# Performance work log

Measured on AMD Instinct MI355X. Metric: run time of the kernel, lower is better.

Reference implementation:

```python
import jax, jax.numpy as jnp
import numpy as np

N_NODES = 100000
N_EDGES = 1600000
N_GRAPHS = 1024
DIM_IN = 128
DIM_SELF = 16
BN_EPS = 1e-5


def _bn(x, gamma, beta):
    # training-mode BatchNorm1d over dim 0 (biased variance, as torch uses for normalization)
    m = jnp.mean(x, axis=0)
    v = jnp.mean((x - m) ** 2, axis=0)
    return gamma * (x - m) * jax.lax.rsqrt(v + BN_EPS) + beta


def _mlp(x, W1, b1, g, b, W2, b2):
    h = x @ W1 + b1
    h = jax.nn.relu(_bn(h, g, b))
    return h @ W2 + b2


def _gin(h, src, dst, W1, b1, g, b, W2, b2):
    # GINConv with eps=0: (1+eps)*h + sum over in-neighbors, then MLP
    agg = jax.ops.segment_sum(h[src], dst, num_segments=N_NODES)
    return _mlp(h + agg, W1, b1, g, b, W2, b2)


def setup_inputs() -> dict:
    key = jax.random.key(0)
    ks = jax.random.split(key, 16)

    def lin(k, fan_in, fan_out):
        bound = 1.0 / np.sqrt(fan_in)
        k1, k2 = jax.random.split(k)
        W = jax.random.uniform(k1, (fan_in, fan_out), jnp.float32, -bound, bound)
        b = jax.random.uniform(k2, (fan_out,), jnp.float32, -bound, bound)
        return W, b

    inp = {}
    inp['feat'] = jax.random.normal(ks[0], (N_NODES, DIM_IN), jnp.float32)
    inp['self_feat'] = jax.random.normal(ks[1], (N_GRAPHS, DIM_SELF), jnp.float32)
    inp['edge_src'] = jax.random.randint(ks[2], (N_EDGES,), 0, N_NODES, jnp.int32)
    inp['edge_dst'] = jax.random.randint(ks[3], (N_EDGES,), 0, N_NODES, jnp.int32)
    inp['node2graph'] = jnp.sort(jax.random.randint(ks[4], (N_NODES,), 0, N_GRAPHS, jnp.int32))

    inp['g1_W1'], inp['g1_b1'] = lin(ks[5], DIM_IN, 100)
    inp['g1_gamma'] = jnp.ones((100,), jnp.float32)
    inp['g1_beta'] = jnp.zeros((100,), jnp.float32)
    inp['g1_W2'], inp['g1_b2'] = lin(ks[6], 100, 100)

    inp['g2_W1'], inp['g2_b1'] = lin(ks[7], 100, 20)
    inp['g2_gamma'] = jnp.ones((20,), jnp.float32)
    inp['g2_beta'] = jnp.zeros((20,), jnp.float32)
    inp['g2_W2'], inp['g2_b2'] = lin(ks[8], 20, 20)

    inp['fc1_W'], inp['fc1_b'] = lin(ks[9], 20 * DIM_SELF, 32)
    inp['bn1_gamma'] = jnp.ones((32,), jnp.float32)
    inp['bn1_beta'] = jnp.zeros((32,), jnp.float32)
    inp['fc2_W'], inp['fc2_b'] = lin(ks[10], 32, 8)
    inp['bn2_gamma'] = jnp.ones((8,), jnp.float32)
    inp['bn2_beta'] = jnp.zeros((8,), jnp.float32)
    inp['fc3_W'], inp['fc3_b'] = lin(ks[11], 8, 1)
    return inp


def reference(feat, self_feat,
              g1_W1, g1_b1, g1_gamma, g1_beta, g1_W2, g1_b2,
              g2_W1, g2_b1, g2_gamma, g2_beta, g2_W2, g2_b2,
              fc1_W, fc1_b, bn1_gamma, bn1_beta,
              fc2_W, fc2_b, bn2_gamma, bn2_beta,
              fc3_W, fc3_b,
              edge_src, edge_dst, node2graph):
    h = _gin(feat, edge_src, edge_dst, g1_W1, g1_b1, g1_gamma, g1_beta, g1_W2, g1_b2)
    h = jax.nn.relu(h)
    h = _gin(h, edge_src, edge_dst, g2_W1, g2_b1, g2_gamma, g2_beta, g2_W2, g2_b2)
    h = jax.nn.relu(h)  # [N, 20]

    # dgl.mean_nodes: per-graph mean of node features
    sums = jax.ops.segment_sum(h, node2graph, num_segments=N_GRAPHS)  # [B, 20]
    cnts = jax.ops.segment_sum(jnp.ones((N_NODES,), h.dtype), node2graph, num_segments=N_GRAPHS)
    hg = sums / jnp.maximum(cnts, 1.0)[:, None]

    # kronecker fusion: bmm([B,20,1],[B,1,dim_self]) -> flatten
    kron = jnp.einsum('bi,bj->bij', hg, self_feat).reshape(N_GRAPHS, -1)  # [B, 20*dim_self]

    out = jax.nn.relu(_bn(kron @ fc1_W + fc1_b, bn1_gamma, bn1_beta))
    # dropout(0.3) is identity in eval mode
    out = jax.nn.relu(_bn(out @ fc2_W + fc2_b, bn2_gamma, bn2_beta))
    out = out @ fc3_W + fc3_b  # [B, dim_out]
    return out
```

## Files before the change

kernel.cpp:

```cpp
#include <hip/hip_runtime.h>

#define NN 100000
#define NE 1600000
#define NG 1024
#define DIN 128
#define D1 100
#define D2 20
#define DSELF 16
#define BN_EPS 1e-5f

#define NB 391
#define NBLK 782
#define EPB 2048
#define RAWCAP 5120
#define NAGG2 4000
#define NF1 25
#define NF2 40
#define APITCH 136

typedef unsigned int uint;
typedef unsigned short ushort;
typedef __attribute__((ext_vector_type(8))) short bfv8;
typedef __attribute__((ext_vector_type(4))) float fv4;

__device__ inline float bflo(uint x) { return __uint_as_float(x << 16); }
__device__ inline float bfhi(uint x) { return __uint_as_float(x & 0xffff0000u); }
__device__ inline uint packbf2(float a, float b) {
    uint ua = __float_as_uint(a), ub = __float_as_uint(b);
    ua += 0x7fffu + ((ua >> 16) & 1u);
    ub += 0x7fffu + ((ub >> 16) & 1u);
    return (ua >> 16) | (ub & 0xffff0000u);
}
__device__ inline ushort bfr(float x) {
    uint u = __float_as_uint(x);
    u += 0x7fffu + ((u >> 16) & 1u);
    return (ushort)(u >> 16);
}

__global__ __launch_bounds__(256) void k_gemm1(const float* __restrict__ feat,
                                               const float* __restrict__ W1,
                                               ushort* __restrict__ z1bf) {
    __shared__ __align__(16) char smem[64 * APITCH * 2 + 112 * APITCH * 2];
    ushort* Al = (ushort*)smem;
    ushort* Bt = (ushort*)(smem + 64 * APITCH * 2);
    int t = threadIdx.x;
    int row0 = blockIdx.x * 64;
#pragma unroll
    for (int i = 0; i < 8; i++) {
        int p = i * 256 + t;
        int r = p >> 5, cq = p & 31;
        int row = row0 + r; if (row >= NN) row = NN - 1;
        float4 v = *(const float4*)(feat + (size_t)row * DIN + cq * 4);
        ushort* dst = Al + r * APITCH + 4 * cq;
        dst[0] = bfr(v.x); dst[1] = bfr(v.y); dst[2] = bfr(v.z); dst[3] = bfr(v.w);
    }
    for (int p = t; p < 12800; p += 256) {
        int k = p / 100, n = p % 100;
        Bt[n * APITCH + k] = bfr(W1[p]);
    }
    __syncthreads();
    int w = __builtin_amdgcn_readfirstlane(t >> 6);
    int l = t & 63;
    int m16 = l & 15, quad = l >> 4;
    fv4 acc[7];
#pragma unroll
    for (int nt = 0; nt < 7; nt++) acc[nt] = (fv4){0.f, 0.f, 0.f, 0.f};
    const ushort* arow = Al + (w * 16 + m16) * APITCH;
#pragma unroll
    for (int kk = 0; kk < 4; kk++) {
        int kb = kk * 32 + quad * 8;
        bfv8 a = *(const bfv8*)(arow + kb);
#pragma unroll
        for (int nt = 0; nt < 7; nt++) {
            bfv8 b = *(const bfv8*)(Bt + (nt * 16 + m16) * APITCH + kb);
            acc[nt] = __builtin_amdgcn_mfma_f32_16x16x32_bf16(a, b, acc[nt], 0, 0, 0);
        }
    }
    __syncthreads();
    float* Ep = (float*)smem;
#pragma unroll
    for (int nt = 0; nt < 7; nt++) {
        int n = nt * 16 + m16;
        if (n < 100) {
#pragma unroll
            for (int rix = 0; rix < 4; rix++)
                Ep[(w * 16 + quad * 4 + rix) * 101 + n] = acc[nt][rix];
        }
    }
    __syncthreads();
#pragma unroll
    for (int i = 0; i < 13; i++) {
        int p = i * 256 + t;
        if (p < 3200) {
            int rr = p / 50, cc = 2 * (p % 50);
            int row = row0 + rr;
            if (row < NN) {
                float v0 = Ep[rr * 101 + cc], v1 = Ep[rr * 101 + cc + 1];
                *(uint*)(z1bf + (size_t)row * 128 + cc) = packbf2(v0, v1);
            }
        }
    }
}

__global__ __launch_bounds__(256) void k_csrA1(const int* __restrict__ dst,
                                               int* __restrict__ pbcount) {
    __shared__ int h[NB];
    int t = threadIdx.x, blk = blockIdx.x;
    for (int i = t; i < NB; i += 256) h[i] = 0;
    __syncthreads();
    int e0 = blk * EPB + t;
#pragma unroll
    for (int i = 0; i < 8; i++) {
        int e = e0 + i * 256;
        if (e < NE) atomicAdd(&h[dst[e] >> 8], 1);
    }
    __syncthreads();
    for (int i = t; i < NB; i += 256) pbcount[i * NBLK + blk] = h[i];
}

__global__ __launch_bounds__(1024) void k_csrS1(int* __restrict__ pbcount,
                                                int* __restrict__ btot) {
    __shared__ int s[1024];
    int t = threadIdx.x, b = blockIdx.x;
    int v = (t < NBLK) ? pbcount[b * NBLK + t] : 0;
    s[t] = v;
    __syncthreads();
    for (int off = 1; off < 1024; off <<= 1) {
        int x = (t >= off) ? s[t - off] : 0;
        __syncthreads();
        s[t] += x;
        __syncthreads();
    }
    if (t < NBLK) pbcount[b * NBLK + t] = s[t] - v;
    if (t == 1023) btot[b] = s[t];
}

__global__ __launch_bounds__(512) void k_csrS2(const int* __restrict__ btot,
                                               int* __restrict__ ebase) {
    __shared__ int s[512];
    int t = threadIdx.x;
    int v = (t < NB) ? btot[t] : 0;
    s[t] = v;
    __syncthreads();
    for (int off = 1; off < 512; off <<= 1) {
        int x = (t >= off) ? s[t - off] : 0;
        __syncthreads();
        s[t] += x;
        __syncthreads();
    }
    if (t < NB) ebase[t] = s[t] - v;
    if (t == NB - 1) ebase[NB] = s[t];
}

__global__ __launch_bounds__(256) void k_csrA2(const int* __restrict__ src,
                                               const int* __restrict__ dst,
                                               const int* __restrict__ pbexcl,
                                               const int* __restrict__ ebase,
                                               uint* __restrict__ gbuf) {
    __shared__ int cur[NB];
    int t = threadIdx.x, blk = blockIdx.x;
    for (int i = t; i < NB; i += 256) cur[i] = ebase[i] + pbexcl[i * NBLK + blk];
    __syncthreads();
    int e0 = blk * EPB + t;
#pragma unroll
    for (int i = 0; i < 8; i++) {
        int e = e0 + i * 256;
        if (e < NE) {
            int d = dst[e];
            int b = d >> 8;
            int pos = atomicAdd(&cur[b], 1);
            gbuf[pos] = (uint)src[e] | ((uint)(d & 255) << 17);
        }
    }
}

__global__ __launch_bounds__(256) void k_csrB(const uint* __restrict__ gbuf,
                                              const int* __restrict__ ebase,
                                              int* __restrict__ deg,
                                              int* __restrict__ offs,
                                              int* __restrict__ srcS) {
    __shared__ uint raw[RAWCAP];
    __shared__ int srt[RAWCAP];
    __shared__ int pref[256], cur[256];
    int t = threadIdx.x, b = blockIdx.x;
    int e0 = ebase[b], e1 = ebase[b + 1];
    int cnt = e1 - e0; if (cnt > RAWCAP) cnt = RAWCAP;
    cur[t] = 0;
    for (int i = t; i < cnt; i += 256) raw[i] = gbuf[e0 + i];
    __syncthreads();
    for (int i = t; i < cnt; i += 256) atomicAdd(&cur[raw[i] >> 17], 1);
    __syncthreads();
    int v = cur[t];
    pref[t] = v;
    __syncthreads();
    for (int off = 1; off < 256; off <<= 1) {
        int x = (t >= off) ? pref[t - off] : 0;
        __syncthreads();
        pref[t] += x;
        __syncthreads();
    }
    int excl = pref[t] - v;
    int node = b * 256 + t;
    if (node < NN) { deg[node] = v; offs[node] = e0 + excl; }
    cur[t] = excl;
    __syncthreads();
    for (int i = t; i < cnt; i += 256) {
        uint p = raw[i];
        int lpos = atomicAdd(&cur[p >> 17], 1);
        srt[lpos] = (int)(p & 0x1FFFFu);
    }
    __syncthreads();
    for (int i = t; i < cnt; i += 256) srcS[e0 + i] = srt[i];
}

__global__ __launch_bounds__(256) void k_agg1(const ushort* __restrict__ z1bf,
                                              const int* __restrict__ offs,
                                              const int* __restrict__ deg,
                                              const int* __restrict__ srcS,
                                              ushort* __restrict__ u1b) {
    int wq = __builtin_amdgcn_readfirstlane(threadIdx.x >> 6);
    int l = threadIdx.x & 63;
    int n = blockIdx.x * 4 + wq;
    if (n >= NN) return;
    int d = deg[n], base = offs[n];
    bool act = l < 50;
    const ushort* zc = z1bf + 2 * l;
    float a0 = 0.f, a1 = 0.f, b0 = 0.f, b1 = 0.f;
    float c0 = 0.f, c1 = 0.f, e0 = 0.f, e1 = 0.f;
    int i = 0;
    for (; i + 4 <= d; i += 4) {
        int s0 = srcS[base + i],     s1 = srcS[base + i + 1];
        int s2 = srcS[base + i + 2], s3 = srcS[base + i + 3];
        if (act) {
            uint x0 = *(const uint*)(zc + (size_t)s0 * 128);
            uint x1 = *(const uint*)(zc + (size_t)s1 * 128);
            uint x2 = *(const uint*)(zc + (size_t)s2 * 128);
            uint x3 = *(const uint*)(zc + (size_t)s3 * 128);
            a0 += bflo(x0); a1 += bfhi(x0);
            b0 += bflo(x1); b1 += bfhi(x1);
            c0 += bflo(x2); c1 += bfhi(x2);
            e0 += bflo(x3); e1 += bfhi(x3);
        }
    }
    for (; i < d; i++) {
        int s0 = srcS[base + i];
        if (act) {
            uint x0 = *(const uint*)(zc + (size_t)s0 * 128);
            a0 += bflo(x0); a1 += bfhi(x0);
        }
    }
    if (act) {
        uint xs = *(const uint*)(zc + (size_t)n * 128);
        float r0 = (a0 + b0) + (c0 + e0) + bflo(xs);
        float r1 = (a1 + b1) + (c1 + e1) + bfhi(xs);
        *(uint*)(u1b + (size_t)n * 100 + 2 * l) = packbf2(r0, r1);
    }
}

__global__ __launch_bounds__(256) void k_bnstat100(const ushort* __restrict__ u1b,
                                                   float* __restrict__ pb) {
    __shared__ float ls[10][100], lq[10][100];
    int t = threadIdx.x;
    int r0 = blockIdx.x * 200;
    int r1 = r0 + 200; if (r1 > NN) r1 = NN;
    if (t < 250) {
        int sub = t / 25, q = t % 25;
        float4 S = make_float4(0, 0, 0, 0), Q = make_float4(0, 0, 0, 0);
        for (int r = r0 + sub; r < r1; r += 10) {
            uint2 x = *(const uint2*)(u1b + (size_t)r * 100 + 4 * q);
            float v0 = bflo(x.x), v1 = bfhi(x.x), v2 = bflo(x.y), v3 = bfhi(x.y);
            S.x += v0; S.y += v1; S.z += v2; S.w += v3;
            Q.x = fmaf(v0, v0, Q.x); Q.y = fmaf(v1, v1, Q.y);
            Q.z = fmaf(v2, v2, Q.z); Q.w = fmaf(v3, v3, Q.w);
        }
        ls[sub][4 * q + 0] = S.x; ls[sub][4 * q + 1] = S.y;
        ls[sub][4 * q + 2] = S.z; ls[sub][4 * q + 3] = S.w;
        lq[sub][4 * q + 0] = Q.x; lq[sub][4 * q + 1] = Q.y;
        lq[sub][4 * q + 2] = Q.z; lq[sub][4 * q + 3] = Q.w;
    }
    __syncthreads();
    if (t < 100) {
        float S = 0.f, Q = 0.f;
#pragma unroll
        for (int s = 0; s < 10; s++) { S += ls[s][t]; Q += lq[s][t]; }
        pb[blockIdx.x * 200 + t] = S;
        pb[blockIdx.x * 200 + 100 + t] = Q;
    }
}

__global__ __launch_bounds__(256) void k_fold100(const float* __restrict__ pb,
                                                 float* __restrict__ pbf) {
    __shared__ float ls[4000];
    int t = threadIdx.x, b = blockIdx.x;
    for (int i = t; i < 4000; i += 256) ls[i] = pb[b * 4000 + i];
    __syncthreads();
    if (t < 200) {
        float S = 0.f;
#pragma unroll
        for (int j = 0; j < 20; j++) S += ls[j * 200 + t];
        pbf[b * 200 + t] = S;
    }
}

__global__ __launch_bounds__(512) void k_bnfin100(const float* __restrict__ pbf,
                                                  const float* __restrict__ gamma,
                                                  const float* __restrict__ beta,
                                                  float* __restrict__ sc,
                                                  float* __restrict__ sh) {
    __shared__ float ls[4][100], lq[4][100];
    int t = threadIdx.x;
    if (t < 400) {
        int sub = t / 100, c = t % 100;
        float S = 0.f, Q = 0.f;
        for (int b = sub; b < NF1; b += 4) {
            S += pbf[b * 200 + c];
            Q += pbf[b * 200 + 100 + c];
        }
        ls[sub][c] = S; lq[sub][c] = Q;
    }
    __syncthreads();
    if (t < 100) {
        float S = ls[0][t] + ls[1][t] + ls[2][t] + ls[3][t];
        float Q = lq[0][t] + lq[1][t] + lq[2][t] + lq[3][t];
        float mean = S * (1.f / NN);
        float var = Q * (1.f / NN) - mean * mean;
        float inv = rsqrtf(var + BN_EPS);
        float s = gamma[t] * inv;
        sc[t] = s;
        sh[t] = beta[t] - mean * s;
    }
}

__global__ __launch_bounds__(256) void k_m2(const ushort* __restrict__ u1b,
                                            const float* __restrict__ sc,
                                            const float* __restrict__ sh,
                                            const float* __restrict__ W2,
                                            const float* __restrict__ b2,
                                            const float* __restrict__ W1p,
                                            ushort* __restrict__ z2bf) {
    __shared__ float Xs[100 * 65];
    int t = threadIdx.x;
    int row0 = blockIdx.x * 64;
#pragma unroll
    for (int i = 0; i < 13; i++) {
        int p = i * 256 + t;
        if (p < 3200) {
            int r = p / 50, c = 2 * (p % 50);
            int row = row0 + r; if (row >= NN) row = NN - 1;
            uint x = *(const uint*)(u1b + (size_t)row * 100 + c);
            Xs[c * 65 + r] = fmaxf(bflo(x) * sc[c] + sh[c], 0.f);
            Xs[(c + 1) * 65 + r] = fmaxf(bfhi(x) * sc[c + 1] + sh[c + 1], 0.f);
        }
    }
    __syncthreads();
    int cg = __builtin_amdgcn_readfirstlane(t >> 6);
    int r = t & 63;
    int j0 = cg * 25;
    float H[25];
#pragma unroll
    for (int m = 0; m < 25; m++) H[m] = 0.f;
    for (int k = 0; k < D1; k++) {
        float a = Xs[k * 65 + r];
        const float* wr = W2 + k * D1 + j0;
#pragma unroll
        for (int m = 0; m < 25; m++) H[m] = fmaf(a, wr[m], H[m]);
    }
#pragma unroll
    for (int m = 0; m < 25; m++) H[m] = fmaxf(H[m] + b2[j0 + m], 0.f);
    float pz[20];
#pragma unroll
    for (int c = 0; c < 20; c++) pz[c] = 0.f;
#pragma unroll
    for (int m = 0; m < 25; m++) {
        const float* wp = W1p + (j0 + m) * D2;
#pragma unroll
        for (int c = 0; c < 20; c++) pz[c] = fmaf(H[m], wp[c], pz[c]);
    }
    __syncthreads();
    float* red = Xs;
#pragma unroll
    for (int c = 0; c < 20; c++) red[t * 20 + c] = pz[c];
    __syncthreads();
#pragma unroll
    for (int i = 0; i < 3; i++) {
        int p = i * 256 + t;
        if (p < 640) {
            int rr = p / 10, c2 = 2 * (p % 10);
            int row = row0 + rr;
            if (row < NN) {
                float v0 = red[rr * 20 + c2] + red[(64 + rr) * 20 + c2] +
                           red[(128 + rr) * 20 + c2] + red[(192 + rr) * 20 + c2];
                float v1 = red[rr * 20 + c2 + 1] + red[(64 + rr) * 20 + c2 + 1] +
                           red[(128 + rr) * 20 + c2 + 1] + red[(192 + rr) * 20 + c2 + 1];
                *(uint*)(z2bf + (size_t)row * 32 + c2) = packbf2(v0, v1);
            }
        }
    }
}

__global__ __launch_bounds__(256) void k_agg2(const ushort* __restrict__ z2bf,
                                              const int* __restrict__ offs,
                                              const int* __restrict__ deg,
                                              const int* __restrict__ srcS,
                                              float* __restrict__ u2,
                                              float* __restrict__ pb) {
    __shared__ float ls[500], lq[500];
    int t = threadIdx.x;
    int n = blockIdx.x * 25 + t / 10;
    int c2 = 2 * (t % 10);
    float r0 = 0.f, r1 = 0.f;
    if (t < 250 && n < NN) {
        int d = deg[n], base = offs[n];
        const ushort* zc = z2bf + c2;
        float a0 = 0.f, a1 = 0.f, b0 = 0.f, b1 = 0.f;
        int i = 0;
        for (; i + 2 <= d; i += 2) {
            uint x0 = *(const uint*)(zc + (size_t)srcS[base + i] * 32);
            uint x1 = *(const uint*)(zc + (size_t)srcS[base + i + 1] * 32);
            a0 += bflo(x0); a1 += bfhi(x0);
            b0 += bflo(x1); b1 += bfhi(x1);
        }
        if (i < d) {
            uint x0 = *(const uint*)(zc + (size_t)srcS[base + i] * 32);
            a0 += bflo(x0); a1 += bfhi(x0);
        }
        uint xs = *(const uint*)(zc + (size_t)n * 32);
        r0 = a0 + b0 + bflo(xs);
        r1 = a1 + b1 + bfhi(xs);
        *(float2*)(u2 + (size_t)n * D2 + c2) = make_float2(r0, r1);
    }
    if (t < 250) {
        int idx = (t / 10) * 20 + c2;
        ls[idx] = r0;     lq[idx] = r0 * r0;
        ls[idx + 1] = r1; lq[idx + 1] = r1 * r1;
    }
    __syncthreads();
    if (t < 20) {
        float S = 0.f, Q = 0.f;
#pragma unroll
        for (int j = 0; j < 25; j++) { S += ls[j * 20 + t]; Q += lq[j * 20 + t]; }
        pb[blockIdx.x * 40 + t] = S;
        pb[blockIdx.x * 40 + 20 + t] = Q;
    }
}

__global__ __launch_bounds__(256) void k_fold20(const float* __restrict__ pb,
                                                float* __restrict__ pbf) {
    __shared__ float ls[4000];
    int t = threadIdx.x, b = blockIdx.x;
    for (int i = t; i < 4000; i += 256) ls[i] = pb[b * 4000 + i];
    __syncthreads();
    if (t < 40) {
        float S = 0.f;
#pragma unroll
        for (int j = 0; j < 100; j++) S += ls[j * 40 + t];
        pbf[b * 40 + t] = S;
    }
}

__global__ __launch_bounds__(512) void k_bnfin20(const float* __restrict__ pbf,
                                                 const float* __restrict__ gamma,
                                                 const float* __restrict__ beta,
                                                 float* __restrict__ sc,
                                                 float* __restrict__ sh) {
    __shared__ float ls[25][20], lq[25][20];
    int t = threadIdx.x;
    if (t < 500) {
        int sub = t / 20, c = t % 20;
        float S = 0.f, Q = 0.f;
        for (int b = sub; b < NF2; b += 25) {
            S += pbf[b * 40 + c];
            Q += pbf[b * 40 + 20 + c];
        }
        ls[sub][c] = S; lq[sub][c] = Q;
    }
    __syncthreads();
    if (t < 20) {
        float S = 0.f, Q = 0.f;
#pragma unroll
        for (int s = 0; s < 25; s++) { S += ls[s][t]; Q += lq[s][t]; }
        float mean = S * (1.f / NN);
        float var = Q * (1.f / NN) - mean * mean;
        float inv = rsqrtf(var + BN_EPS);
        float s = gamma[t] * inv;
        sc[t] = s;
        sh[t] = beta[t] - mean * s;
    }
}

__global__ __launch_bounds__(256) void k_m3(const float* __restrict__ u2,
                                            const float* __restrict__ sc,
                                            const float* __restrict__ sh,
                                            const float* __restrict__ W2p,
                                            const float* __restrict__ b2p,
                                            float* __restrict__ h2) {
    int row = blockIdx.x * 256 + threadIdx.x;
    if (row >= NN) return;
    float ya[20];
    const float4* up = (const float4*)(u2 + (size_t)row * D2);
#pragma unroll
    for (int i = 0; i < 5; i++) {
        float4 v = up[i];
        float4 S = *(const float4*)(sc + 4 * i);
        float4 H = *(const float4*)(sh + 4 * i);
        ya[4 * i + 0] = fmaxf(v.x * S.x + H.x, 0.f);
        ya[4 * i + 1] = fmaxf(v.y * S.y + H.y, 0.f);
        ya[4 * i + 2] = fmaxf(v.z * S.z + H.z, 0.f);
        ya[4 * i + 3] = fmaxf(v.w * S.w + H.w, 0.f);
    }
    float hrow[D2];
#pragma unroll
    for (int j = 0; j < D2; j++) {
        float h = b2p[j];
#pragma unroll
        for (int k = 0; k < D2; k++) h = fmaf(ya[k], W2p[k * D2 + j], h);
        hrow[j] = fmaxf(h, 0.f);
    }
    float* hr = h2 + (size_t)row * D2;
#pragma unroll
    for (int c = 0; c < D2; c += 4) {
        float4 o; o.x = hrow[c]; o.y = hrow[c + 1]; o.z = hrow[c + 2]; o.w = hrow[c + 3];
        *(float4*)(hr + c) = o;
    }
}

__global__ __launch_bounds__(256) void k_pool(const float* __restrict__ h2,
                                              const int* __restrict__ n2g,
                                              float* __restrict__ hg) {
    int wq = __builtin_amdgcn_readfirstlane(threadIdx.x >> 6);
    int l = threadIdx.x & 63;
    int g = blockIdx.x * 4 + wq;
    if (g >= NG) return;
    int lo = 0, hi = NN;
    while (lo < hi) { int mid = (lo + hi) >> 1; if (n2g[mid] < g) lo = mid + 1; else hi = mid; }
    int s0 = lo;
    hi = NN;
    while (lo < hi) { int mid = (lo + hi) >> 1; if (n2g[mid] < g + 1) lo = mid + 1; else hi = mid; }
    int s1 = lo;
    float a = 0.f;
    if (l < 60) {
        int rg = l / 20, c = l % 20;
        for (int n = s0 + rg; n < s1; n += 3) a += h2[(size_t)n * D2 + c];
    }
    float v1 = __shfl(a, l + 20, 64);
    float v2 = __shfl(a, l + 40, 64);
    if (l < 20) {
        float cnt = (float)(s1 - s0);
        hg[g * D2 + l] = (a + v1 + v2) / fmaxf(cnt, 1.f);
    }
}

__global__ void k_head1(const float* __restrict__ hg, const float* __restrict__ sf,
                        const float* __restrict__ fc1W, float* __restrict__ a1) {
    int b = blockIdx.x * 8 + threadIdx.x / 32;
    int c = threadIdx.x % 32;
    if (b >= NG) return;
    const float* hgb = hg + b * D2;
    const float* sfb = sf + b * DSELF;
    float acc = 0.f;
    for (int i = 0; i < D2; i++) {
        float hi = hgb[i];
#pragma unroll
        for (int j = 0; j < DSELF; j++)
            acc += hi * sfb[j] * fc1W[(i * DSELF + j) * 32 + c];
    }
    a1[b * 32 + c] = acc;
}

__global__ __launch_bounds__(1024) void k_head2(
    const float* __restrict__ a1, const float* __restrict__ g1,
    const float* __restrict__ be1, const float* __restrict__ fc2W,
    const float* __restrict__ g2, const float* __restrict__ be2,
    const float* __restrict__ fc3W, const float* __restrict__ fc3b,
    float* __restrict__ out) {
    int t = threadIdx.x;
    int lane = t & 63, w = t >> 6;
    __shared__ float s1[16][32], s2[16][32];
    __shared__ float sc[32], sh[32], sc2[8], sh2[8];
    float x[32];
    const float4* ap = (const float4*)(a1 + t * 32);
#pragma unroll
    for (int i = 0; i < 8; i++) {
        float4 v = ap[i];
        x[4 * i] = v.x; x[4 * i + 1] = v.y; x[4 * i + 2] = v.z; x[4 * i + 3] = v.w;
    }
#pragma unroll
    for (int c = 0; c < 32; c++) {
        float v = x[c], q = v * v;
        for (int o = 32; o > 0; o >>= 1) {
            v += __shfl_down(v, o, 64);
            q += __shfl_down(q, o, 64);
        }
        if (lane == 0) { s1[w][c] = v; s2[w][c] = q; }
    }
    __syncthreads();
    if (t < 32) {
        float s = 0.f, q = 0.f;
        for (int ww = 0; ww < 16; ww++) { s += s1[ww][t]; q += s2[ww][t]; }
        float mean = s * (1.f / NG);
        float var = q * (1.f / NG) - mean * mean;
        float inv = rsqrtf(var + BN_EPS);
        float scl = g1[t] * inv;
        sc[t] = scl;
        sh[t] = be1[t] - mean * scl;
    }
    __syncthreads();
#pragma unroll
    for (int c = 0; c < 32; c++) x[c] = fmaxf(x[c] * sc[c] + sh[c], 0.f);
    float y[8];
#pragma unroll
    for (int p = 0; p < 8; p++) {
        float a = 0.f;
#pragma unroll
        for (int c = 0; c < 32; c++) a += x[c] * fc2W[c * 8 + p];
        y[p] = a;
    }
    __syncthreads();
#pragma unroll
    for (int p = 0; p < 8; p++) {
        float v = y[p], q = v * v;
        for (int o = 32; o > 0; o >>= 1) {
            v += __shfl_down(v, o, 64);
            q += __shfl_down(q, o, 64);
        }
        if (lane == 0) { s1[w][p] = v; s2[w][p] = q; }
    }
    __syncthreads();
    if (t < 8) {
        float s = 0.f, q = 0.f;
        for (int ww = 0; ww < 16; ww++) { s += s1[ww][t]; q += s2[ww][t]; }
        float mean = s * (1.f / NG);
        float var = q * (1.f / NG) - mean * mean;
        float inv = rsqrtf(var + BN_EPS);
        float scl = g2[t] * inv;
        sc2[t] = scl;
        sh2[t] = be2[t] - mean * scl;
    }
    __syncthreads();
    float o = fc3b[0];
#pragma unroll
    for (int p = 0; p < 8; p++) {
        float yy = fmaxf(y[p] * sc2[p] + sh2[p], 0.f);
        o += yy * fc3W[p];
    }
    out[t] = o;
}

extern "C" void kernel_launch(void* const* d_in, const int* in_sizes, int n_in,
                              void* d_out, int out_size, void* d_ws, size_t ws_size,
                              hipStream_t stream) {
    const float* feat    = (const float*)d_in[0];
    const float* sf      = (const float*)d_in[1];
    const int*   esrc    = (const int*)d_in[2];
    const int*   edst    = (const int*)d_in[3];
    const int*   n2g     = (const int*)d_in[4];
    const float* g1W1    = (const float*)d_in[5];
    const float* g1gam   = (const float*)d_in[7];
    const float* g1bet   = (const float*)d_in[8];
    const float* g1W2    = (const float*)d_in[9];
    const float* g1b2    = (const float*)d_in[10];
    const float* g2W1    = (const float*)d_in[11];
    const float* g2gam   = (const float*)d_in[13];
    const float* g2bet   = (const float*)d_in[14];
    const float* g2W2    = (const float*)d_in[15];
    const float* g2b2    = (const float*)d_in[16];
    const float* fc1W    = (const float*)d_in[17];
    const float* hbn1g   = (const float*)d_in[19];
    const float* hbn1b   = (const float*)d_in[20];
    const float* fc2W    = (const float*)d_in[21];
    const float* hbn2g   = (const float*)d_in[23];
    const float* hbn2b   = (const float*)d_in[24];
    const float* fc3W    = (const float*)d_in[25];
    const float* fc3b    = (const float*)d_in[26];
    float* out = (float*)d_out;

    char* w = (char*)d_ws;
    size_t off = 0;
    auto alloc = [&](size_t bytes) -> char* {
        char* p = w + off;
        off += (bytes + 15) & ~(size_t)15;
        return p;
    };
    char* regA = alloc((size_t)NN * 128 * 2);
    ushort* z1bf = (ushort*)regA;
    ushort* z2bf = (ushort*)regA;
    float*  u2   = (float*)(regA + 6400000);
    float*  h2   = (float*)(regA + 14400000);
    ushort* u1b  = (ushort*)alloc((size_t)NN * 100 * 2);
    int*   pbcnt = (int*)alloc((size_t)NB * NBLK * 4);
    int*   btot  = (int*)alloc(NB * 4);
    int*   ebase = (int*)alloc((NB + 1) * 4);
    uint*  gbuf  = (uint*)alloc((size_t)NE * 4);
    int*   deg   = (int*)alloc(NN * 4);
    int*   offs  = (int*)alloc(NN * 4);
    int*   srcS  = (int*)alloc((size_t)NE * 4);
    float* pb1   = (float*)alloc(500 * 200 * 4);
    float* pb1f  = (float*)alloc(NF1 * 200 * 4);
    float* pb2   = (float*)alloc((size_t)NAGG2 * 40 * 4);
    float* pb2f  = (float*)alloc(NF2 * 40 * 4);
    float* sc1   = (float*)alloc(D1 * 4);
    float* sh1   = (float*)alloc(D1 * 4);
    float* sc2   = (float*)alloc(D2 * 4);
    float* sh2   = (float*)alloc(D2 * 4);
    float* hg    = (float*)alloc(NG * D2 * 4);
    float* a1    = (float*)alloc(NG * 32 * 4);
    (void)in_sizes; (void)n_in; (void)out_size; (void)ws_size;

    k_gemm1<<<(NN + 63) / 64, 256, 0, stream>>>(feat, g1W1, z1bf);

    k_csrA1<<<NBLK, 256, 0, stream>>>(edst, pbcnt);
    k_csrS1<<<NB, 1024, 0, stream>>>(pbcnt, btot);
    k_csrS2<<<1, 512, 0, stream>>>(btot, ebase);
    k_csrA2<<<NBLK, 256, 0, stream>>>(esrc, edst, pbcnt, ebase, gbuf);
    k_csrB<<<NB, 256, 0, stream>>>(gbuf, ebase, deg, offs, srcS);

    k_agg1<<<(NN + 3) / 4, 256, 0, stream>>>(z1bf, offs, deg, srcS, u1b);
    k_bnstat100<<<500, 256, 0, stream>>>(u1b, pb1);
    k_fold100<<<NF1, 256, 0, stream>>>(pb1, pb1f);
    k_bnfin100<<<1, 512, 0, stream>>>(pb1f, g1gam, g1bet, sc1, sh1);
    k_m2<<<(NN + 63) / 64, 256, 0, stream>>>(u1b, sc1, sh1, g1W2, g1b2, g2W1, z2bf);

    k_agg2<<<NAGG2, 256, 0, stream>>>(z2bf, offs, deg, srcS, u2, pb2);
    k_fold20<<<NF2, 256, 0, stream>>>(pb2, pb2f);
    k_bnfin20<<<1, 512, 0, stream>>>(pb2f, g2gam, g2bet, sc2, sh2);
    k_m3<<<(NN + 255) / 256, 256, 0, stream>>>(u2, sc2, sh2, g2W2, g2b2, h2);

    k_pool<<<(NG + 3) / 4, 256, 0, stream>>>(h2, n2g, hg);
    k_head1<<<NG / 8, 256, 0, stream>>>(hg, sf, fc1W, a1);
    k_head2<<<1, 1024, 0, stream>>>(a1, hbn1g, hbn1b, fc2W, hbn2g, hbn2b, fc3W, fc3b, out);
}
```

Baseline: 450.1 us.

## Fuse kernels to cut launches: gemm+histogram, scans, BN folds, m3+pool+head1

Merges the edge-destination histogram into the first GEMM launch as extra blocks. The second-level bucket scan moves into every csrA2 block, which also writes ebase. The two-stage BN partial folds collapse into single 1024-thread finalize kernels. The m3 MLP, mean pooling and fc1 head are fused into one per-graph kernel, which removes the h2 and hg intermediates. The aim is fewer launches and less global traffic, at the cost of redundant scans per block and a less parallel m3 computation (one wave per graph).

```diff
diff --git a/kernel.cpp b/kernel.cpp
--- a/kernel.cpp
+++ b/kernel.cpp
@@ -11,11 +11,10 @@
 
 #define NB 391
 #define NBLK 782
+#define GEMMB 1563
 #define EPB 2048
 #define RAWCAP 5120
 #define NAGG2 4000
-#define NF1 25
-#define NF2 40
 #define APITCH 136
 
 typedef unsigned int uint;
@@ -37,14 +36,32 @@
     return (ushort)(u >> 16);
 }
 
-__global__ __launch_bounds__(256) void k_gemm1(const float* __restrict__ feat,
-                                               const float* __restrict__ W1,
-                                               ushort* __restrict__ z1bf) {
+__global__ __launch_bounds__(256) void k_fused1(const float* __restrict__ feat,
+                                                const float* __restrict__ W1,
+                                                ushort* __restrict__ z1bf,
+                                                const int* __restrict__ edst,
+                                                int* __restrict__ pbcount) {
     __shared__ __align__(16) char smem[64 * APITCH * 2 + 112 * APITCH * 2];
+    int t = threadIdx.x;
+    int bid = blockIdx.x;
+    if (bid >= GEMMB) {
+        int* h = (int*)smem;
+        int blk = bid - GEMMB;
+        for (int i = t; i < NB; i += 256) h[i] = 0;
+        __syncthreads();
+        int e0 = blk * EPB + t;
+#pragma unroll
+        for (int i = 0; i < 8; i++) {
+            int e = e0 + i * 256;
+            if (e < NE) atomicAdd(&h[edst[e] >> 8], 1);
+        }
+        __syncthreads();
+        for (int i = t; i < NB; i += 256) pbcount[i * NBLK + blk] = h[i];
+        return;
+    }
     ushort* Al = (ushort*)smem;
     ushort* Bt = (ushort*)(smem + 64 * APITCH * 2);
-    int t = threadIdx.x;
-    int row0 = blockIdx.x * 64;
+    int row0 = bid * 64;
 #pragma unroll
     for (int i = 0; i < 8; i++) {
         int p = i * 256 + t;
@@ -102,22 +119,6 @@
     }
 }
 
-__global__ __launch_bounds__(256) void k_csrA1(const int* __restrict__ dst,
-                                               int* __restrict__ pbcount) {
-    __shared__ int h[NB];
-    int t = threadIdx.x, blk = blockIdx.x;
-    for (int i = t; i < NB; i += 256) h[i] = 0;
-    __syncthreads();
-    int e0 = blk * EPB + t;
-#pragma unroll
-    for (int i = 0; i < 8; i++) {
-        int e = e0 + i * 256;
-        if (e < NE) atomicAdd(&h[dst[e] >> 8], 1);
-    }
-    __syncthreads();
-    for (int i = t; i < NB; i += 256) pbcount[i * NBLK + blk] = h[i];
-}
-
 __global__ __launch_bounds__(1024) void k_csrS1(int* __restrict__ pbcount,
                                                 int* __restrict__ btot) {
     __shared__ int s[1024];
@@ -135,31 +136,34 @@
     if (t == 1023) btot[b] = s[t];
 }
 
-__global__ __launch_bounds__(512) void k_csrS2(const int* __restrict__ btot,
-                                               int* __restrict__ ebase) {
-    __shared__ int s[512];
-    int t = threadIdx.x;
-    int v = (t < NB) ? btot[t] : 0;
-    s[t] = v;
-    __syncthreads();
-    for (int off = 1; off < 512; off <<= 1) {
-        int x = (t >= off) ? s[t - off] : 0;
-        __syncthreads();
-        s[t] += x;
-        __syncthreads();
-    }
-    if (t < NB) ebase[t] = s[t] - v;
-    if (t == NB - 1) ebase[NB] = s[t];
-}
-
 __global__ __launch_bounds__(256) void k_csrA2(const int* __restrict__ src,
                                                const int* __restrict__ dst,
                                                const int* __restrict__ pbexcl,
-                                               const int* __restrict__ ebase,
+                                               const int* __restrict__ btot,
+                                               int* __restrict__ ebase_g,
                                                uint* __restrict__ gbuf) {
     __shared__ int cur[NB];
+    __shared__ int sa[512], sb[512];
     int t = threadIdx.x, blk = blockIdx.x;
-    for (int i = t; i < NB; i += 256) cur[i] = ebase[i] + pbexcl[i * NBLK + blk];
+    int o0 = (t < NB) ? btot[t] : 0;
+    int o1 = (t + 256 < NB) ? btot[t + 256] : 0;
+    sa[t] = o0; sa[t + 256] = o1;
+    __syncthreads();
+    int* sp = sa; int* dp = sb;
+    for (int off = 1; off < 512; off <<= 1) {
+        dp[t] = sp[t] + ((t >= off) ? sp[t - off] : 0);
+        int i2 = t + 256;
+        dp[i2] = sp[i2] + ((i2 >= off) ? sp[i2 - off] : 0);
+        __syncthreads();
+        int* tmp = sp; sp = dp; dp = tmp;
+    }
+    if (t < NB)       cur[t]       = (sp[t] - o0) + pbexcl[t * NBLK + blk];
+    if (t + 256 < NB) cur[t + 256] = (sp[t + 256] - o1) + pbexcl[(t + 256) * NBLK + blk];
+    if (blk == 0) {
+        if (t < NB)       ebase_g[t]       = sp[t] - o0;
+        if (t + 256 < NB) ebase_g[t + 256] = sp[t + 256] - o1;
+        if (t == 0)       ebase_g[NB]      = sp[NB - 1];
+    }
     __syncthreads();
     int e0 = blk * EPB + t;
 #pragma unroll
@@ -288,40 +292,27 @@
     }
 }
 
-__global__ __launch_bounds__(256) void k_fold100(const float* __restrict__ pb,
-                                                 float* __restrict__ pbf) {
-    __shared__ float ls[4000];
-    int t = threadIdx.x, b = blockIdx.x;
-    for (int i = t; i < 4000; i += 256) ls[i] = pb[b * 4000 + i];
+__global__ __launch_bounds__(1024) void k_bnfin100(const float* __restrict__ pb,
+                                                   const float* __restrict__ gamma,
+                                                   const float* __restrict__ beta,
+                                                   float* __restrict__ sc,
+                                                   float* __restrict__ sh) {
+    __shared__ float rs[5][200];
+    int t = threadIdx.x;
+    float acc = 0.f;
+    if (t < 1000) {
+        int c = t % 200, sub = t / 200;
+        for (int b = sub; b < 500; b += 5) acc += pb[b * 200 + c];
+        rs[sub][c] = acc;
+    }
     __syncthreads();
     if (t < 200) {
-        float S = 0.f;
-#pragma unroll
-        for (int j = 0; j < 20; j++) S += ls[j * 200 + t];
-        pbf[b * 200 + t] = S;
-    }
-}
-
-__global__ __launch_bounds__(512) void k_bnfin100(const float* __restrict__ pbf,
-                                                  const float* __restrict__ gamma,
-                                                  const float* __restrict__ beta,
-                                                  float* __restrict__ sc,
-                                                  float* __restrict__ sh) {
-    __shared__ float ls[4][100], lq[4][100];
-    int t = threadIdx.x;
-    if (t < 400) {
-        int sub = t / 100, c = t % 100;
-        float S = 0.f, Q = 0.f;
-        for (int b = sub; b < NF1; b += 4) {
-            S += pbf[b * 200 + c];
-            Q += pbf[b * 200 + 100 + c];
-        }
-        ls[sub][c] = S; lq[sub][c] = Q;
+        float S = rs[0][t] + rs[1][t] + rs[2][t] + rs[3][t] + rs[4][t];
+        rs[0][t] = S;
     }
     __syncthreads();
     if (t < 100) {
-        float S = ls[0][t] + ls[1][t] + ls[2][t] + ls[3][t];
-        float Q = lq[0][t] + lq[1][t] + lq[2][t] + lq[3][t];
+        float S = rs[0][t], Q = rs[0][t + 100];
         float mean = S * (1.f / NN);
         float var = Q * (1.f / NN) - mean * mean;
         float inv = rsqrtf(var + BN_EPS);
@@ -444,41 +435,29 @@
     }
 }
 
-__global__ __launch_bounds__(256) void k_fold20(const float* __restrict__ pb,
-                                                float* __restrict__ pbf) {
-    __shared__ float ls[4000];
-    int t = threadIdx.x, b = blockIdx.x;
-    for (int i = t; i < 4000; i += 256) ls[i] = pb[b * 4000 + i];
+__global__ __launch_bounds__(1024) void k_bnfin20(const float* __restrict__ pb,
+                                                  const float* __restrict__ gamma,
+                                                  const float* __restrict__ beta,
+                                                  float* __restrict__ sc,
+                                                  float* __restrict__ sh) {
+    __shared__ float rs[25][40];
+    int t = threadIdx.x;
+    float acc = 0.f;
+    if (t < 1000) {
+        int c = t % 40, sub = t / 40;
+        for (int b = sub; b < NAGG2; b += 25) acc += pb[b * 40 + c];
+        rs[sub][c] = acc;
+    }
     __syncthreads();
     if (t < 40) {
         float S = 0.f;
 #pragma unroll
-        for (int j = 0; j < 100; j++) S += ls[j * 40 + t];
-        pbf[b * 40 + t] = S;
-    }
-}
-
-__global__ __launch_bounds__(512) void k_bnfin20(const float* __restrict__ pbf,
-                                                 const float* __restrict__ gamma,
-                                                 const float* __restrict__ beta,
-                                                 float* __restrict__ sc,
-                                                 float* __restrict__ sh) {
-    __shared__ float ls[25][20], lq[25][20];
-    int t = threadIdx.x;
-    if (t < 500) {
-        int sub = t / 20, c = t % 20;
-        float S = 0.f, Q = 0.f;
-        for (int b = sub; b < NF2; b += 25) {
-            S += pbf[b * 40 + c];
-            Q += pbf[b * 40 + 20 + c];
-        }
-        ls[sub][c] = S; lq[sub][c] = Q;
+        for (int s = 0; s < 25; s++) S += rs[s][t];
+        rs[0][t] = S;
     }
     __syncthreads();
     if (t < 20) {
-        float S = 0.f, Q = 0.f;
-#pragma unroll
-        for (int s = 0; s < 25; s++) { S += ls[s][t]; Q += lq[s][t]; }
+        float S = rs[0][t], Q = rs[0][t + 20];
         float mean = S * (1.f / NN);
         float var = Q * (1.f / NN) - mean * mean;
         float inv = rsqrtf(var + BN_EPS);
@@ -488,45 +467,15 @@
     }
 }
 
-__global__ __launch_bounds__(256) void k_m3(const float* __restrict__ u2,
-                                            const float* __restrict__ sc,
-                                            const float* __restrict__ sh,
-                                            const float* __restrict__ W2p,
-                                            const float* __restrict__ b2p,
-                                            float* __restrict__ h2) {
-    int row = blockIdx.x * 256 + threadIdx.x;
-    if (row >= NN) return;
-    float ya[20];
-    const float4* up = (const float4*)(u2 + (size_t)row * D2);
-#pragma unroll
-    for (int i = 0; i < 5; i++) {
-        float4 v = up[i];
-        float4 S = *(const float4*)(sc + 4 * i);
-        float4 H = *(const float4*)(sh + 4 * i);
-        ya[4 * i + 0] = fmaxf(v.x * S.x + H.x, 0.f);
-        ya[4 * i + 1] = fmaxf(v.y * S.y + H.y, 0.f);
-        ya[4 * i + 2] = fmaxf(v.z * S.z + H.z, 0.f);
-        ya[4 * i + 3] = fmaxf(v.w * S.w + H.w, 0.f);
-    }
-    float hrow[D2];
-#pragma unroll
-    for (int j = 0; j < D2; j++) {
-        float h = b2p[j];
-#pragma unroll
-        for (int k = 0; k < D2; k++) h = fmaf(ya[k], W2p[k * D2 + j], h);
-        hrow[j] = fmaxf(h, 0.f);
-    }
-    float* hr = h2 + (size_t)row * D2;
-#pragma unroll
-    for (int c = 0; c < D2; c += 4) {
-        float4 o; o.x = hrow[c]; o.y = hrow[c + 1]; o.z = hrow[c + 2]; o.w = hrow[c + 3];
-        *(float4*)(hr + c) = o;
-    }
-}
-
-__global__ __launch_bounds__(256) void k_pool(const float* __restrict__ h2,
-                                              const int* __restrict__ n2g,
-                                              float* __restrict__ hg) {
+__global__ __launch_bounds__(256) void k_m3pool(const float* __restrict__ u2,
+                                                const int* __restrict__ n2g,
+                                                const float* __restrict__ sc,
+                                                const float* __restrict__ sh,
+                                                const float* __restrict__ W2p,
+                                                const float* __restrict__ b2p,
+                                                const float* __restrict__ sf,
+                                                const float* __restrict__ fc1W,
+                                                float* __restrict__ a1) {
     int wq = __builtin_amdgcn_readfirstlane(threadIdx.x >> 6);
     int l = threadIdx.x & 63;
     int g = blockIdx.x * 4 + wq;
@@ -537,34 +486,50 @@
     hi = NN;
     while (lo < hi) { int mid = (lo + hi) >> 1; if (n2g[mid] < g + 1) lo = mid + 1; else hi = mid; }
     int s1 = lo;
-    float a = 0.f;
+    float accp = 0.f;
     if (l < 60) {
         int rg = l / 20, c = l % 20;
-        for (int n = s0 + rg; n < s1; n += 3) a += h2[(size_t)n * D2 + c];
-    }
-    float v1 = __shfl(a, l + 20, 64);
-    float v2 = __shfl(a, l + 40, 64);
-    if (l < 20) {
-        float cnt = (float)(s1 - s0);
-        hg[g * D2 + l] = (a + v1 + v2) / fmaxf(cnt, 1.f);
-    }
-}
-
-__global__ void k_head1(const float* __restrict__ hg, const float* __restrict__ sf,
-                        const float* __restrict__ fc1W, float* __restrict__ a1) {
-    int b = blockIdx.x * 8 + threadIdx.x / 32;
-    int c = threadIdx.x % 32;
-    if (b >= NG) return;
-    const float* hgb = hg + b * D2;
-    const float* sfb = sf + b * DSELF;
-    float acc = 0.f;
-    for (int i = 0; i < D2; i++) {
-        float hi = hgb[i];
-#pragma unroll
-        for (int j = 0; j < DSELF; j++)
-            acc += hi * sfb[j] * fc1W[(i * DSELF + j) * 32 + c];
-    }
-    a1[b * 32 + c] = acc;
+        float wcol[20];
+#pragma unroll
+        for (int k = 0; k < 20; k++) wcol[k] = W2p[k * 20 + c];
+        float bc = b2p[c];
+        for (int n = s0 + rg; n < s1; n += 3) {
+            const float4* ur = (const float4*)(u2 + (size_t)n * 20);
+            float h = bc;
+#pragma unroll
+            for (int q = 0; q < 5; q++) {
+                float4 v = ur[q];
+                float4 S = *(const float4*)(sc + 4 * q);
+                float4 H = *(const float4*)(sh + 4 * q);
+                h = fmaf(fmaxf(v.x * S.x + H.x, 0.f), wcol[4 * q + 0], h);
+                h = fmaf(fmaxf(v.y * S.y + H.y, 0.f), wcol[4 * q + 1], h);
+                h = fmaf(fmaxf(v.z * S.z + H.z, 0.f), wcol[4 * q + 2], h);
+                h = fmaf(fmaxf(v.w * S.w + H.w, 0.f), wcol[4 * q + 3], h);
+            }
+            accp += fmaxf(h, 0.f);
+        }
+    }
+    float v1 = __shfl(accp, l + 20, 64);
+    float v2 = __shfl(accp, l + 40, 64);
+    float hgq = 0.f;
+    float cnt = fmaxf((float)(s1 - s0), 1.f);
+    if (l < 20) hgq = (accp + v1 + v2) / cnt;
+    float sfv[16];
+    const float* sfb = sf + g * DSELF;
+#pragma unroll
+    for (int j = 0; j < 16; j++) sfv[j] = sfb[j];
+    float acc1 = 0.f;
+#pragma unroll
+    for (int i = 0; i < 20; i++) {
+        float hgi = __shfl(hgq, i, 64);
+        if (l < 32) {
+            const float* wrow = fc1W + i * DSELF * 32 + l;
+#pragma unroll
+            for (int j = 0; j < 16; j++)
+                acc1 = fmaf(hgi * sfv[j], wrow[j * 32], acc1);
+        }
+    }
+    if (l < 32) a1[g * 32 + l] = acc1;
 }
 
 __global__ __launch_bounds__(1024) void k_head2(
@@ -685,7 +650,6 @@
     ushort* z1bf = (ushort*)regA;
     ushort* z2bf = (ushort*)regA;
     float*  u2   = (float*)(regA + 6400000);
-    float*  h2   = (float*)(regA + 14400000);
     ushort* u1b  = (ushort*)alloc((size_t)NN * 100 * 2);
     int*   pbcnt = (int*)alloc((size_t)NB * NBLK * 4);
     int*   btot  = (int*)alloc(NB * 4);
@@ -695,37 +659,25 @@
     int*   offs  = (int*)alloc(NN * 4);
     int*   srcS  = (int*)alloc((size_t)NE * 4);
     float* pb1   = (float*)alloc(500 * 200 * 4);
-    float* pb1f  = (float*)alloc(NF1 * 200 * 4);
     float* pb2   = (float*)alloc((size_t)NAGG2 * 40 * 4);
-    float* pb2f  = (float*)alloc(NF2 * 40 * 4);
     float* sc1   = (float*)alloc(D1 * 4);
     float* sh1   = (float*)alloc(D1 * 4);
     float* sc2   = (float*)alloc(D2 * 4);
     float* sh2   = (float*)alloc(D2 * 4);
-    float* hg    = (float*)alloc(NG * D2 * 4);
     float* a1    = (float*)alloc(NG * 32 * 4);
     (void)in_sizes; (void)n_in; (void)out_size; (void)ws_size;
 
-    k_gemm1<<<(NN + 63) / 64, 256, 0, stream>>>(feat, g1W1, z1bf);
-
-    k_csrA1<<<NBLK, 256, 0, stream>>>(edst, pbcnt);
+    k_fused1<<<GEMMB + NBLK, 256, 0, stream>>>(feat, g1W1, z1bf, edst, pbcnt);
     k_csrS1<<<NB, 1024, 0, stream>>>(pbcnt, btot);
-    k_csrS2<<<1, 512, 0, stream>>>(btot, ebase);
-    k_csrA2<<<NBLK, 256, 0, stream>>>(esrc, edst, pbcnt, ebase, gbuf);
+    k_csrA2<<<NBLK, 256, 0, stream>>>(esrc, edst, pbcnt, btot, ebase, gbuf);
     k_csrB<<<NB, 256, 0, stream>>>(gbuf, ebase, deg, offs, srcS);
-
     k_agg1<<<(NN + 3) / 4, 256, 0, stream>>>(z1bf, offs, deg, srcS, u1b);
     k_bnstat100<<<500, 256, 0, stream>>>(u1b, pb1);
-    k_fold100<<<NF1, 256, 0, stream>>>(pb1, pb1f);
-    k_bnfin100<<<1, 512, 0, stream>>>(pb1f, g1gam, g1bet, sc1, sh1);
+    k_bnfin100<<<1, 1024, 0, stream>>>(pb1, g1gam, g1bet, sc1, sh1);
     k_m2<<<(NN + 63) / 64, 256, 0, stream>>>(u1b, sc1, sh1, g1W2, g1b2, g2W1, z2bf);
-
     k_agg2<<<NAGG2, 256, 0, stream>>>(z2bf, offs, deg, srcS, u2, pb2);
-    k_fold20<<<NF2, 256, 0, stream>>>(pb2, pb2f);
-    k_bnfin20<<<1, 512, 0, stream>>>(pb2f, g2gam, g2bet, sc2, sh2);
-    k_m3<<<(NN + 255) / 256, 256, 0, stream>>>(u2, sc2, sh2, g2W2, g2b2, h2);
-
-    k_pool<<<(NG + 3) / 4, 256, 0, stream>>>(h2, n2g, hg);
-    k_head1<<<NG / 8, 256, 0, stream>>>(hg, sf, fc1W, a1);
+    k_bnfin20<<<1, 1024, 0, stream>>>(pb2, g2gam, g2bet, sc2, sh2);
+    k_m3pool<<<(NG + 3) / 4, 256, 0, stream>>>(u2, n2g, sc2, sh2, g2W2, g2b2,
+                                               sf, fc1W, a1);
     k_head2<<<1, 1024, 0, stream>>>(a1, hbn1g, hbn1b, fc2W, hbn2g, hbn2b, fc3W, fc3b, out);
 }
```

Result: slower. 479.0 us (+6.4%).
